# Kernel tuning notes

Measured on AMD Instinct MI355X. Metric: run time of the kernel, lower is better.

The kernel has to match this reference:

```python
import jax, jax.numpy as jnp
import numpy as np

EMBED = 1024
HEADS = 16


def setup_inputs() -> dict:
    key = jax.random.key(0)
    k1, k2, k3 = jax.random.split(key, 3)
    b, n, e = 2, 2048, EMBED
    x = jax.random.normal(k1, (b, n, e), dtype=jnp.float32)
    # torch nn.Linear stores weight as [out_features, in_features]
    w_qkv = jax.random.normal(k2, (3 * e, e), dtype=jnp.float32) * (1.0 / np.sqrt(e))
    w_proj = jax.random.normal(k3, (e, e), dtype=jnp.float32) * (1.0 / np.sqrt(e))
    b_proj = jnp.zeros((e,), dtype=jnp.float32)
    return {"x": x, "w_qkv": w_qkv, "w_proj": w_proj, "b_proj": b_proj}


def reference(x, w_qkv, w_proj, b_proj):
    b, n, e = x.shape
    h = HEADS
    d = e // h
    # qkv: [b, n, 3e]; einops 'b n (h d qkv)' -> qkv index is innermost
    qkv = jnp.einsum('bne,fe->bnf', x, w_qkv).reshape(b, n, h, d, 3)
    # -> [b, h, n, d] each
    q = jnp.transpose(qkv[..., 0], (0, 2, 1, 3))
    k = jnp.transpose(qkv[..., 1], (0, 2, 1, 3))
    v = jnp.transpose(qkv[..., 2], (0, 2, 1, 3))
    energy = jnp.einsum('bhqd,bhkd->bhqk', q, k)
    # NOTE: original applies softmax first, THEN divides by sqrt(embed_size)
    scaling = jnp.asarray(e, dtype=x.dtype) ** 0.5
    att = jax.nn.softmax(energy, axis=-1) / scaling
    out = jnp.einsum('bhqk,bhkd->bhqd', att, v)
    out = jnp.transpose(out, (0, 2, 1, 3)).reshape(b, n, e)
    proj = jnp.einsum('bne,fe->bnf', out, w_proj) + b_proj
    return jax.nn.relu(proj)
```

## Files before the change

### kernel.cpp

```cpp
#include <hip/hip_runtime.h>
#include <math.h>

constexpr int EMBED = 1024;
constexpr int HEADS = 16;
constexpr int HDIM  = 64;
constexpr int BATCH = 2;
constexpr int SEQ   = 2048;
constexpr int MTOT  = BATCH * SEQ;
constexpr int LDA   = 1024;
constexpr int BHSZ  = SEQ * HDIM;

typedef unsigned short u16;
using f16x8  = __attribute__((ext_vector_type(8))) short;
using f32x4  = __attribute__((ext_vector_type(4))) float;
using f32x16 = __attribute__((ext_vector_type(16))) float;
using u32x4  = __attribute__((ext_vector_type(4))) unsigned int;

__device__ __forceinline__ u16 f2bf(float f) {
    unsigned u = __builtin_bit_cast(unsigned, f);
    return (u16)((u + 0x7fffu + ((u >> 16) & 1u)) >> 16);
}
__device__ __forceinline__ u16 f2h(float f) {
    _Float16 h = (_Float16)f;
    return __builtin_bit_cast(u16, h);
}
__device__ __forceinline__ unsigned cvtpk(float lo, float hi) {
    unsigned r;
    asm("v_cvt_pk_bf16_f32 %0, %1, %2" : "=v"(r) : "v"(lo), "v"(hi));
    return r;
}
__device__ __forceinline__ float exp2i(float x) {
    float r;
    asm("v_exp_f32 %0, %1" : "=v"(r) : "v"(x));
    return r;
}

#define GLOAD16(gp, lp) __builtin_amdgcn_global_load_lds( \
    (const __attribute__((address_space(1))) unsigned int*)(gp), \
    (__attribute__((address_space(3))) unsigned int*)(lp), 16, 0, 0)

__global__ __launch_bounds__(256)
void convert_split(const float* __restrict__ X, const float* __restrict__ Wq,
                   const float* __restrict__ Wp,
                   u16* __restrict__ Xs, u16* __restrict__ Wqs, u16* __restrict__ Wps)
{
    int m = blockIdx.x;
    int k = threadIdx.x * 4;
    const float* src; u16* dst;
    if (m < 4096) {
        src = X + (size_t)m * EMBED;          dst = Xs + (size_t)m * LDA;
    } else if (m < 7168) {
        int f = m - 4096;
        int h = f / 192, rem = f - h * 192, d = rem / 3, wq = rem - d * 3;
        int nrow = wq * 1024 + h * 64 + d;
        src = Wq + (size_t)f * EMBED;         dst = Wqs + (size_t)nrow * LDA;
    } else {
        int lm = m - 7168;
        src = Wp + (size_t)lm * EMBED;        dst = Wps + (size_t)lm * LDA;
    }
    float4 v = *(const float4*)(src + k);
    ushort4 hv;
    hv.x = f2h(v.x); hv.y = f2h(v.y); hv.z = f2h(v.z); hv.w = f2h(v.w);
    *(ushort4*)(dst + k) = hv;
}

__device__ __forceinline__ void stage4(
    const u16* __restrict__ A, const u16* __restrict__ B,
    u16* SHu, int buf, int kt, int tid)
{
    const int k0 = kt * 32;
    u16* dst = SHu + buf * 16384;
    #pragma unroll
    for (int i = 0; i < 2; ++i) {
        const int s    = i * 512 + tid;
        const int row  = s >> 2;
        const int gcol = ((s & 3) ^ ((row >> 1) & 3)) * 8;
        GLOAD16(A + (size_t)row * LDA + k0 + gcol, dst + s * 8);
        GLOAD16(B + (size_t)row * LDA + k0 + gcol, dst + 8192 + s * 8);
    }
}

__global__ __launch_bounds__(512)
void gemm_qkv_pipe(const u16* __restrict__ Xs, const u16* __restrict__ Wqs,
                   u16* __restrict__ Qh, u16* __restrict__ Kh,
                   u16* __restrict__ Vt)
{
    __shared__ __align__(16) u16 SHu[65536];
    const int bid = blockIdx.x;
    const int xcd = bid & 7, j = bid >> 3;
    const int bm  = xcd * 2 + (j & 1);
    const int bn  = j >> 1;
    const int tid = threadIdx.x, wid = tid >> 6, lane = tid & 63;
    const int wr  = wid >> 2, wc = wid & 3;

    const u16* Ab = Xs  + (size_t)bm * 256 * LDA;
    const u16* Bb = Wqs + (size_t)bn * 256 * LDA;

    const int frow = lane & 15;
    const int kg8s = ((lane >> 4) ^ ((lane >> 1) & 3)) * 8;

    f32x4 acc[8][4] = {};

    stage4(Ab, Bb, SHu, 0, 0, tid);
    stage4(Ab, Bb, SHu, 1, 1, tid);
    stage4(Ab, Bb, SHu, 2, 2, tid);
    asm volatile("s_waitcnt vmcnt(8)" ::: "memory");
    __builtin_amdgcn_s_barrier();

    for (int kt = 0; kt < 32; ++kt) {
        const u16* bufp = SHu + (kt & 3) * 16384;
        f16x8 bf[4], af[8];
        #pragma unroll
        for (int ni = 0; ni < 4; ++ni)
            bf[ni] = *(const f16x8*)&bufp[8192 + (wc * 64 + ni * 16 + frow) * 32 + kg8s];
        #pragma unroll
        for (int mi = 0; mi < 8; ++mi)
            af[mi] = *(const f16x8*)&bufp[(wr * 128 + mi * 16 + frow) * 32 + kg8s];
        if (kt + 3 < 32) stage4(Ab, Bb, SHu, (kt + 3) & 3, kt + 3, tid);
        __builtin_amdgcn_s_setprio(1);
        #pragma unroll
        for (int mi = 0; mi < 8; ++mi)
            #pragma unroll
            for (int ni = 0; ni < 4; ++ni)
                acc[mi][ni] = __builtin_amdgcn_mfma_f32_16x16x32_f16(
                    af[mi], bf[ni], acc[mi][ni], 0, 0, 0);
        __builtin_amdgcn_s_setprio(0);
        asm volatile("s_waitcnt lgkmcnt(0)" ::: "memory");
        if (kt <= 28) { asm volatile("s_waitcnt vmcnt(8)" ::: "memory"); }
        else          { asm volatile("s_waitcnt vmcnt(0)" ::: "memory"); }
        __builtin_amdgcn_s_barrier();
    }

    const int f_base = bn * 256 + wc * 64;
    const int which  = f_base >> 10;
    const int h      = (f_base >> 6) & 15;
    char* T = (char*)(SHu + wid * 8192);
    constexpr float RCP_LN2 = 1.4426950408889634f;

    #pragma unroll
    for (int hp = 0; hp < 2; ++hp) {
        const int ng  = bm * 256 + wr * 128 + hp * 64;
        const int b_  = ng >> 11;
        const int n0w = ng & 2047;
        const size_t bhb = (size_t)(b_ * HEADS + h) * BHSZ;

        if (which < 2) {
            const float qs = (which == 0) ? RCP_LN2 : 1.0f;
            u16* dst = (which == 0 ? Qh : Kh) + bhb;
            #pragma unroll
            for (int mi = 0; mi < 4; ++mi)
                #pragma unroll
                for (int ni = 0; ni < 4; ++ni)
                    #pragma unroll
                    for (int r = 0; r < 4; ++r) {
                        u16 ov = f2h(acc[hp * 4 + mi][ni][r] * qs);
                        int nl = ((lane >> 4) << 2) + mi * 16 + r;
                        int dl = ni * 16 + (lane & 15);
                        *(u16*)(T + nl * 128 + ((dl * 2) ^ ((nl & 7) << 4))) = ov;
                    }
            #pragma unroll
            for (int t2 = 0; t2 < 2; ++t2)
                #pragma unroll
                for (int dt = 0; dt < 4; ++dt) {
                    int nl   = t2 * 32 + (lane & 31);
                    int doff = (dt * 16 + (lane >> 5) * 8) * 2;
                    f16x8 fr = *(const f16x8*)(T + nl * 128 + (doff ^ ((nl & 7) << 4)));
                    int tile = (n0w >> 5) + t2;
                    *(f16x8*)&dst[(size_t)(tile * 4 + dt) * 512 + lane * 8] = fr;
                }
        } else {
            #pragma unroll
            for (int mi = 0; mi < 4; ++mi)
                #pragma unroll
                for (int ni = 0; ni < 4; ++ni)
                    #pragma unroll
                    for (int r = 0; r < 4; ++r) {
                        int nl = ((lane >> 4) << 2) + mi * 16 + r;
                        int dl = ni * 16 + (lane & 15);
                        *(u16*)(T + nl * 128 + ((dl * 2) ^ ((nl & 7) << 4))) =
                            f2bf(acc[hp * 4 + mi][ni][r]);
                    }
            u16* dst = Vt + bhb;
            #pragma unroll
            for (int t2 = 0; t2 < 2; ++t2)
                #pragma unroll
                for (int dtv = 0; dtv < 2; ++dtv)
                    #pragma unroll
                    for (int kt2 = 0; kt2 < 2; ++kt2) {
                        int dcol = (dtv * 32 + (lane & 31)) * 2;
                        int nb   = t2 * 32 + kt2 * 16 + (lane >> 5) * 8;
                        f16x8 fr;
                        #pragma unroll
                        for (int j2 = 0; j2 < 8; ++j2) {
                            int nl = nb + j2;
                            fr[j2] = *(const short*)(T + nl * 128 + (dcol ^ ((nl & 7) << 4)));
                        }
                        int tile = (n0w >> 5) + t2;
                        *(f16x8*)&dst[(size_t)(((tile * 2 + dtv) * 2 + kt2) * 64 + lane) * 8] = fr;
                    }
        }
    }
}

__device__ __forceinline__ void stage_pf(
    const u16* __restrict__ A, const u16* __restrict__ B,
    u16* As, u16* Bs, int buf, int t, int wid, int lane)
{
    const int k0 = t * 32;
    const int srow = lane >> 2;
    const int sc   = (((lane & 3) ^ ((lane >> 3) & 3))) * 8;
    u16* ab = As + buf * 4096;
    u16* bb = Bs + buf * 4096;
    #pragma unroll
    for (int i = 0; i < 2; ++i) {
        const int rb = wid * 32 + i * 16;
        GLOAD16(A + (size_t)(rb + srow) * LDA + k0 + sc, ab + rb * 32);
        GLOAD16(B + (size_t)(rb + srow) * LDA + k0 + sc, bb + rb * 32);
    }
}

__device__ __forceinline__ void mfma_loop_pf(
    const u16* __restrict__ Ab, const u16* __restrict__ Bb,
    u16* As, u16* Bs, f32x4 (&acc)[4][4], int wid, int lane)
{
    constexpr int NT = 32;
    const int wr = wid >> 1, wc = wid & 1;
    const int frow = lane & 15;
    const int kg8s = (((lane >> 4) ^ ((lane >> 1) & 3))) * 8;

    stage_pf(Ab, Bb, As, Bs, 0, 0, wid, lane);
    stage_pf(Ab, Bb, As, Bs, 1, 1, wid, lane);
    asm volatile("s_waitcnt vmcnt(4)" ::: "memory");
    __builtin_amdgcn_s_barrier();
    __builtin_amdgcn_sched_barrier(0);

    int cb = 0, sb = 2;
    for (int t = 0; t < NT; ++t) {
        if (t + 2 < NT) stage_pf(Ab, Bb, As, Bs, sb, t + 2, wid, lane);
        const u16* ap = As + cb * 4096;
        const u16* bp = Bs + cb * 4096;
        f16x8 a[4], b[4];
        #pragma unroll
        for (int mi = 0; mi < 4; ++mi)
            a[mi] = *(const f16x8*)&ap[(wr * 64 + mi * 16 + frow) * 32 + kg8s];
        #pragma unroll
        for (int ni = 0; ni < 4; ++ni)
            b[ni] = *(const f16x8*)&bp[(wc * 64 + ni * 16 + frow) * 32 + kg8s];
        #pragma unroll
        for (int mi = 0; mi < 4; ++mi)
            #pragma unroll
            for (int ni = 0; ni < 4; ++ni)
                acc[mi][ni] = __builtin_amdgcn_mfma_f32_16x16x32_f16(
                    a[mi], b[ni], acc[mi][ni], 0, 0, 0);
        __builtin_amdgcn_sched_barrier(0);
        asm volatile("s_waitcnt lgkmcnt(0)" ::: "memory");
        if (t + 2 < NT) { asm volatile("s_waitcnt vmcnt(4)" ::: "memory"); }
        else            { asm volatile("s_waitcnt vmcnt(0)" ::: "memory"); }
        __builtin_amdgcn_s_barrier();
        __builtin_amdgcn_sched_barrier(0);
        cb = cb == 2 ? 0 : cb + 1;
        sb = sb == 2 ? 0 : sb + 1;
    }
}

__global__ __launch_bounds__(256)
void gemm_proj_mfma(const u16* __restrict__ CTXs, const u16* __restrict__ Wps,
                    const float* __restrict__ bias, float* __restrict__ Out)
{
    __shared__ __align__(16) u16 SH[6 * 4096];
    const int bid = blockIdx.x;
    const int xcd = bid & 7, j = bid >> 3;
    const int bm  = xcd * 4 + (j & 3);
    const int bn  = j >> 2;
    const int wid = threadIdx.x >> 6, lane = threadIdx.x & 63;
    const int wr = wid >> 1, wc = wid & 1;

    f32x4 acc[4][4] = {};
    mfma_loop_pf(CTXs + (size_t)bm * 128 * LDA, Wps + (size_t)bn * 128 * LDA,
                 SH, SH + 3 * 4096, acc, wid, lane);

    const int m0 = bm * 128 + wr * 64 + ((lane >> 4) << 2);
    #pragma unroll
    for (int ni = 0; ni < 4; ++ni) {
        const int f  = bn * 128 + wc * 64 + ni * 16 + (lane & 15);
        const float bv = bias[f];
        #pragma unroll
        for (int mi = 0; mi < 4; ++mi) {
            const int m = m0 + mi * 16;
            #pragma unroll
            for (int r = 0; r < 4; ++r)
                Out[(size_t)(m + r) * EMBED + f] = fmaxf(acc[mi][ni][r] + bv, 0.f);
        }
    }
}

__device__ __forceinline__ void attn_body(
    int t, int tend,
    const u16* __restrict__ vb, const u16* __restrict__ kb,
    f16x8 (&kfc)[4], f16x8 (&kfn)[4],
    f16x8 (&vfc)[4], f16x8 (&vfn)[4],
    const f16x8 (&qf)[4],
    f32x16& ot0, f32x16& ot1, float& l_run)
{
    if (t + 1 < tend) {
        #pragma unroll
        for (int dt = 0; dt < 4; ++dt)
            kfn[dt] = *(const f16x8*)(kb + (size_t)(t + 1) * 2048 + dt * 512);
        #pragma unroll
        for (int dt = 0; dt < 2; ++dt)
            #pragma unroll
            for (int kt = 0; kt < 2; ++kt)
                vfn[dt * 2 + kt] = *(const f16x8*)(vb + (size_t)(t + 1) * 2048 + dt * 1024 + kt * 512);
    }

    f32x16 st = {-16.f, -16.f, -16.f, -16.f, -16.f, -16.f, -16.f, -16.f,
                 -16.f, -16.f, -16.f, -16.f, -16.f, -16.f, -16.f, -16.f};
    #pragma unroll
    for (int dt = 0; dt < 4; ++dt)
        st = __builtin_amdgcn_mfma_f32_32x32x16_f16(kfc[dt], qf[dt], st, 0, 0, 0);

    float p[16];
    #pragma unroll
    for (int r = 0; r < 16; ++r) p[r] = exp2i(st[r]);
    {
        float s0 = (p[0] + p[1]) + (p[2] + p[3]);
        float s1 = (p[4] + p[5]) + (p[6] + p[7]);
        float s2 = (p[8] + p[9]) + (p[10] + p[11]);
        float s3 = (p[12] + p[13]) + (p[14] + p[15]);
        l_run += (s0 + s1) + (s2 + s3);
    }

    unsigned W0 = cvtpk(p[0],  p[1]),  W1 = cvtpk(p[2],  p[3]);
    unsigned W2 = cvtpk(p[4],  p[5]),  W3 = cvtpk(p[6],  p[7]);
    unsigned W4 = cvtpk(p[8],  p[9]),  W5 = cvtpk(p[10], p[11]);
    unsigned W6 = cvtpk(p[12], p[13]), W7 = cvtpk(p[14], p[15]);
    asm("v_permlane32_swap_b32 %0, %1" : "+v"(W0), "+v"(W2));
    asm("v_permlane32_swap_b32 %0, %1" : "+v"(W1), "+v"(W3));
    asm("v_permlane32_swap_b32 %0, %1" : "+v"(W4), "+v"(W6));
    asm("v_permlane32_swap_b32 %0, %1" : "+v"(W5), "+v"(W7));
    u32x4 u0 = {W0, W1, W2, W3};
    u32x4 u1 = {W4, W5, W6, W7};
    f16x8 pf0 = __builtin_bit_cast(f16x8, u0);
    f16x8 pf1 = __builtin_bit_cast(f16x8, u1);

    ot0 = __builtin_amdgcn_mfma_f32_32x32x16_bf16(vfc[0], pf0, ot0, 0, 0, 0);
    ot1 = __builtin_amdgcn_mfma_f32_32x32x16_bf16(vfc[2], pf0, ot1, 0, 0, 0);
    ot0 = __builtin_amdgcn_mfma_f32_32x32x16_bf16(vfc[1], pf1, ot0, 0, 0, 0);
    ot1 = __builtin_amdgcn_mfma_f32_32x32x16_bf16(vfc[3], pf1, ot1, 0, 0, 0);
}

__global__ __launch_bounds__(256)
void attn_mfma(const u16* __restrict__ Qh, const u16* __restrict__ Kh,
               const u16* __restrict__ Vt,  u16* __restrict__ CTXs)
{
    __shared__ __align__(16) float Lot[2][64][33];
    __shared__ float Lml[2][32];
    __shared__ __align__(16) float Ol[2][32][68];

    const int bid  = blockIdx.x;
    const int swz  = (bid & 7) * 128 + (bid >> 3);
    const int bh   = swz >> 5;
    const int qp   = swz & 31;
    const int wid  = threadIdx.x >> 6;
    const int lane = threadIdx.x & 63;
    const int col  = lane & 31;
    const int g    = lane >> 5;
    const int qt   = wid >> 1;
    const int kh   = wid & 1;

    const int q0   = qp * 64 + qt * 32;
    const int b_   = bh / HEADS;
    const int h    = bh % HEADS;
    const int tbeg = kh * (SEQ / 2 / 32);
    const int tend = tbeg + SEQ / 2 / 32;

    const size_t bhb = (size_t)bh * BHSZ;
    const u16* kb = Kh + bhb + (size_t)lane * 8;
    const u16* vb = Vt + bhb + (size_t)lane * 8;

    f16x8 qf[4];
    {
        const u16* qbh = Qh + bhb + (size_t)(q0 >> 5) * 2048 + (size_t)lane * 8;
        #pragma unroll
        for (int dt = 0; dt < 4; ++dt)
            qf[dt] = *(const f16x8*)(qbh + dt * 512);
    }

    f32x16 ot0 = {}, ot1 = {};
    float l_run = 0.0f;

    f16x8 kfA[4], kfB[4], vfA[4], vfB[4];
    #pragma unroll
    for (int dt = 0; dt < 4; ++dt)
        kfA[dt] = *(const f16x8*)(kb + (size_t)tbeg * 2048 + dt * 512);
    #pragma unroll
    for (int dt = 0; dt < 2; ++dt)
        #pragma unroll
        for (int kt = 0; kt < 2; ++kt)
            vfA[dt * 2 + kt] = *(const f16x8*)(vb + (size_t)tbeg * 2048 + dt * 1024 + kt * 512);

    for (int t = tbeg; t < tend; t += 2) {
        attn_body(t,     tend, vb, kb, kfA, kfB, vfA, vfB, qf, ot0, ot1, l_run);
        attn_body(t + 1, tend, vb, kb, kfB, kfA, vfB, vfA, qf, ot0, ot1, l_run);
    }

    l_run += __shfl_xor(l_run, 32);

    if (kh == 1) {
        #pragma unroll
        for (int r = 0; r < 16; ++r) {
            int d = (r & 3) + 8 * (r >> 2) + 4 * g;
            Lot[qt][d][col]      = ot0[r];
            Lot[qt][d + 32][col] = ot1[r];
        }
        if (g == 0) Lml[qt][col] = l_run;
    }
    __syncthreads();
    if (kh == 0) {
        float l  = l_run + Lml[qt][col];
        float sc = 1.0f / (l * 32.0f);
        #pragma unroll
        for (int r = 0; r < 16; ++r) {
            int d = (r & 3) + 8 * (r >> 2) + 4 * g;
            Ol[qt][col][d]      = (ot0[r] + Lot[qt][d][col]) * sc;
            Ol[qt][col][d + 32] = (ot1[r] + Lot[qt][d + 32][col]) * sc;
        }
        #pragma unroll
        for (int pass = 0; pass < 8; ++pass) {
            int qq = pass * 4 + (lane >> 4);
            int dd = (lane & 15) * 4;
            float4 t = *(const float4*)&Ol[qt][qq][dd];
            int m_ = b_ * SEQ + q0 + qq;
            ushort4 hv;
            hv.x = f2h(t.x); hv.y = f2h(t.y);
            hv.z = f2h(t.z); hv.w = f2h(t.w);
            *(ushort4*)&CTXs[(size_t)m_ * LDA + h * HDIM + dd] = hv;
        }
    }
}

extern "C" void kernel_launch(void* const* d_in, const int* in_sizes, int n_in,
                              void* d_out, int out_size, void* d_ws, size_t ws_size,
                              hipStream_t stream)
{
    const float* x      = (const float*)d_in[0];
    const float* w_qkv  = (const float*)d_in[1];
    const float* w_proj = (const float*)d_in[2];
    const float* b_proj = (const float*)d_in[3];
    float* out = (float*)d_out;

    const size_t seg = (size_t)BATCH * HEADS * SEQ * HDIM;
    char* w = (char*)d_ws;
    u16* Xs   = (u16*)w;  w += (size_t)MTOT * LDA * 2;
    u16* Wqs  = (u16*)w;  w += (size_t)3 * EMBED * LDA * 2;
    u16* Wps  = (u16*)w;  w += (size_t)EMBED * LDA * 2;
    u16* Qh   = (u16*)w;  w += seg * 2;
    u16* Kh   = (u16*)w;  w += seg * 2;
    u16* Vt   = (u16*)w;  w += seg * 2;
    u16* CTXs = Xs;

    convert_split<<<dim3(8192), 256, 0, stream>>>(x, w_qkv, w_proj, Xs, Wqs, Wps);
    gemm_qkv_pipe<<<dim3(192), 512, 0, stream>>>(Xs, Wqs, Qh, Kh, Vt);
    attn_mfma<<<dim3(1024), 256, 0, stream>>>(Qh, Kh, Vt, CTXs);
    gemm_proj_mfma<<<dim3(256), 256, 0, stream>>>(CTXs, Wps, b_proj, out);
}
```

Measured before the change: 112.3 us.

## Process two query tiles per attention wave to reuse K/V fragments

Each attention wave now computes scores and outputs for two 32-query tiles against the same K and V fragments, so each K/V global load is reused twice. The grid is halved to 512 blocks and the block-to-(head, query) swizzle is adjusted. The split-K reduction epilogue runs twice with extra barriers. This doubles accumulator and Q register usage and halves the number of blocks, which can lower occupancy and latency hiding.

```diff
diff --git a/kernel.cpp b/kernel.cpp
--- a/kernel.cpp
+++ b/kernel.cpp
@@ -299,8 +299,9 @@
     const u16* __restrict__ vb, const u16* __restrict__ kb,
     f16x8 (&kfc)[4], f16x8 (&kfn)[4],
     f16x8 (&vfc)[4], f16x8 (&vfn)[4],
-    const f16x8 (&qf)[4],
-    f32x16& ot0, f32x16& ot1, float& l_run)
+    const f16x8 (&qfa)[4], const f16x8 (&qfb)[4],
+    f32x16& oa0, f32x16& oa1, f32x16& ob0, f32x16& ob1,
+    float& la, float& lb)
 {
     if (t + 1 < tend) {
         #pragma unroll
@@ -313,40 +314,63 @@
                 vfn[dt * 2 + kt] = *(const f16x8*)(vb + (size_t)(t + 1) * 2048 + dt * 1024 + kt * 512);
     }
 
-    f32x16 st = {-16.f, -16.f, -16.f, -16.f, -16.f, -16.f, -16.f, -16.f,
-                 -16.f, -16.f, -16.f, -16.f, -16.f, -16.f, -16.f, -16.f};
-    #pragma unroll
-    for (int dt = 0; dt < 4; ++dt)
-        st = __builtin_amdgcn_mfma_f32_32x32x16_f16(kfc[dt], qf[dt], st, 0, 0, 0);
-
-    float p[16];
-    #pragma unroll
-    for (int r = 0; r < 16; ++r) p[r] = exp2i(st[r]);
+    const f32x16 minit = {-16.f, -16.f, -16.f, -16.f, -16.f, -16.f, -16.f, -16.f,
+                          -16.f, -16.f, -16.f, -16.f, -16.f, -16.f, -16.f, -16.f};
+    f32x16 sta = minit, stb = minit;
+    #pragma unroll
+    for (int dt = 0; dt < 4; ++dt) {
+        sta = __builtin_amdgcn_mfma_f32_32x32x16_f16(kfc[dt], qfa[dt], sta, 0, 0, 0);
+        stb = __builtin_amdgcn_mfma_f32_32x32x16_f16(kfc[dt], qfb[dt], stb, 0, 0, 0);
+    }
+
+    f16x8 pa0, pa1, pb0, pb1;
     {
-        float s0 = (p[0] + p[1]) + (p[2] + p[3]);
-        float s1 = (p[4] + p[5]) + (p[6] + p[7]);
-        float s2 = (p[8] + p[9]) + (p[10] + p[11]);
-        float s3 = (p[12] + p[13]) + (p[14] + p[15]);
-        l_run += (s0 + s1) + (s2 + s3);
-    }
-
-    unsigned W0 = cvtpk(p[0],  p[1]),  W1 = cvtpk(p[2],  p[3]);
-    unsigned W2 = cvtpk(p[4],  p[5]),  W3 = cvtpk(p[6],  p[7]);
-    unsigned W4 = cvtpk(p[8],  p[9]),  W5 = cvtpk(p[10], p[11]);
-    unsigned W6 = cvtpk(p[12], p[13]), W7 = cvtpk(p[14], p[15]);
-    asm("v_permlane32_swap_b32 %0, %1" : "+v"(W0), "+v"(W2));
-    asm("v_permlane32_swap_b32 %0, %1" : "+v"(W1), "+v"(W3));
-    asm("v_permlane32_swap_b32 %0, %1" : "+v"(W4), "+v"(W6));
-    asm("v_permlane32_swap_b32 %0, %1" : "+v"(W5), "+v"(W7));
-    u32x4 u0 = {W0, W1, W2, W3};
-    u32x4 u1 = {W4, W5, W6, W7};
-    f16x8 pf0 = __builtin_bit_cast(f16x8, u0);
-    f16x8 pf1 = __builtin_bit_cast(f16x8, u1);
-
-    ot0 = __builtin_amdgcn_mfma_f32_32x32x16_bf16(vfc[0], pf0, ot0, 0, 0, 0);
-    ot1 = __builtin_amdgcn_mfma_f32_32x32x16_bf16(vfc[2], pf0, ot1, 0, 0, 0);
-    ot0 = __builtin_amdgcn_mfma_f32_32x32x16_bf16(vfc[1], pf1, ot0, 0, 0, 0);
-    ot1 = __builtin_amdgcn_mfma_f32_32x32x16_bf16(vfc[3], pf1, ot1, 0, 0, 0);
+        float p[16];
+        #pragma unroll
+        for (int r = 0; r < 16; ++r) p[r] = exp2i(sta[r]);
+        la += ((p[0] + p[1]) + (p[2] + p[3])) + ((p[4] + p[5]) + (p[6] + p[7]))
+            + ((p[8] + p[9]) + (p[10] + p[11])) + ((p[12] + p[13]) + (p[14] + p[15]));
+        unsigned W0 = cvtpk(p[0],  p[1]),  W1 = cvtpk(p[2],  p[3]);
+        unsigned W2 = cvtpk(p[4],  p[5]),  W3 = cvtpk(p[6],  p[7]);
+        unsigned W4 = cvtpk(p[8],  p[9]),  W5 = cvtpk(p[10], p[11]);
+        unsigned W6 = cvtpk(p[12], p[13]), W7 = cvtpk(p[14], p[15]);
+        asm("v_permlane32_swap_b32 %0, %1" : "+v"(W0), "+v"(W2));
+        asm("v_permlane32_swap_b32 %0, %1" : "+v"(W1), "+v"(W3));
+        asm("v_permlane32_swap_b32 %0, %1" : "+v"(W4), "+v"(W6));
+        asm("v_permlane32_swap_b32 %0, %1" : "+v"(W5), "+v"(W7));
+        u32x4 u0 = {W0, W1, W2, W3};
+        u32x4 u1 = {W4, W5, W6, W7};
+        pa0 = __builtin_bit_cast(f16x8, u0);
+        pa1 = __builtin_bit_cast(f16x8, u1);
+    }
+    {
+        float p[16];
+        #pragma unroll
+        for (int r = 0; r < 16; ++r) p[r] = exp2i(stb[r]);
+        lb += ((p[0] + p[1]) + (p[2] + p[3])) + ((p[4] + p[5]) + (p[6] + p[7]))
+            + ((p[8] + p[9]) + (p[10] + p[11])) + ((p[12] + p[13]) + (p[14] + p[15]));
+        unsigned W0 = cvtpk(p[0],  p[1]),  W1 = cvtpk(p[2],  p[3]);
+        unsigned W2 = cvtpk(p[4],  p[5]),  W3 = cvtpk(p[6],  p[7]);
+        unsigned W4 = cvtpk(p[8],  p[9]),  W5 = cvtpk(p[10], p[11]);
+        unsigned W6 = cvtpk(p[12], p[13]), W7 = cvtpk(p[14], p[15]);
+        asm("v_permlane32_swap_b32 %0, %1" : "+v"(W0), "+v"(W2));
+        asm("v_permlane32_swap_b32 %0, %1" : "+v"(W1), "+v"(W3));
+        asm("v_permlane32_swap_b32 %0, %1" : "+v"(W4), "+v"(W6));
+        asm("v_permlane32_swap_b32 %0, %1" : "+v"(W5), "+v"(W7));
+        u32x4 u0 = {W0, W1, W2, W3};
+        u32x4 u1 = {W4, W5, W6, W7};
+        pb0 = __builtin_bit_cast(f16x8, u0);
+        pb1 = __builtin_bit_cast(f16x8, u1);
+    }
+
+    oa0 = __builtin_amdgcn_mfma_f32_32x32x16_bf16(vfc[0], pa0, oa0, 0, 0, 0);
+    oa1 = __builtin_amdgcn_mfma_f32_32x32x16_bf16(vfc[2], pa0, oa1, 0, 0, 0);
+    ob0 = __builtin_amdgcn_mfma_f32_32x32x16_bf16(vfc[0], pb0, ob0, 0, 0, 0);
+    ob1 = __builtin_amdgcn_mfma_f32_32x32x16_bf16(vfc[2], pb0, ob1, 0, 0, 0);
+    oa0 = __builtin_amdgcn_mfma_f32_32x32x16_bf16(vfc[1], pa1, oa0, 0, 0, 0);
+    oa1 = __builtin_amdgcn_mfma_f32_32x32x16_bf16(vfc[3], pa1, oa1, 0, 0, 0);
+    ob0 = __builtin_amdgcn_mfma_f32_32x32x16_bf16(vfc[1], pb1, ob0, 0, 0, 0);
+    ob1 = __builtin_amdgcn_mfma_f32_32x32x16_bf16(vfc[3], pb1, ob1, 0, 0, 0);
 }
 
 __global__ __launch_bounds__(256)
@@ -358,9 +382,9 @@
     __shared__ __align__(16) float Ol[2][32][68];
 
     const int bid  = blockIdx.x;
-    const int swz  = (bid & 7) * 128 + (bid >> 3);
-    const int bh   = swz >> 5;
-    const int qp   = swz & 31;
+    const int swz  = (bid & 7) * 64 + (bid >> 3);
+    const int bh   = swz >> 4;
+    const int qp   = swz & 15;
     const int wid  = threadIdx.x >> 6;
     const int lane = threadIdx.x & 63;
     const int col  = lane & 31;
@@ -368,7 +392,7 @@
     const int qt   = wid >> 1;
     const int kh   = wid & 1;
 
-    const int q0   = qp * 64 + qt * 32;
+    const int q0   = qp * 128 + qt * 64;
     const int b_   = bh / HEADS;
     const int h    = bh % HEADS;
     const int tbeg = kh * (SEQ / 2 / 32);
@@ -378,16 +402,18 @@
     const u16* kb = Kh + bhb + (size_t)lane * 8;
     const u16* vb = Vt + bhb + (size_t)lane * 8;
 
-    f16x8 qf[4];
+    f16x8 qfa[4], qfb[4];
     {
-        const u16* qbh = Qh + bhb + (size_t)(q0 >> 5) * 2048 + (size_t)lane * 8;
-        #pragma unroll
-        for (int dt = 0; dt < 4; ++dt)
-            qf[dt] = *(const f16x8*)(qbh + dt * 512);
-    }
-
-    f32x16 ot0 = {}, ot1 = {};
-    float l_run = 0.0f;
+        const u16* qb0 = Qh + bhb + (size_t)(q0 >> 5) * 2048 + (size_t)lane * 8;
+        #pragma unroll
+        for (int dt = 0; dt < 4; ++dt) {
+            qfa[dt] = *(const f16x8*)(qb0 + dt * 512);
+            qfb[dt] = *(const f16x8*)(qb0 + 2048 + dt * 512);
+        }
+    }
+
+    f32x16 oa0 = {}, oa1 = {}, ob0 = {}, ob1 = {};
+    float la = 0.0f, lb = 0.0f;
 
     f16x8 kfA[4], kfB[4], vfA[4], vfB[4];
     #pragma unroll
@@ -400,41 +426,49 @@
             vfA[dt * 2 + kt] = *(const f16x8*)(vb + (size_t)tbeg * 2048 + dt * 1024 + kt * 512);
 
     for (int t = tbeg; t < tend; t += 2) {
-        attn_body(t,     tend, vb, kb, kfA, kfB, vfA, vfB, qf, ot0, ot1, l_run);
-        attn_body(t + 1, tend, vb, kb, kfB, kfA, vfB, vfA, qf, ot0, ot1, l_run);
-    }
-
-    l_run += __shfl_xor(l_run, 32);
-
-    if (kh == 1) {
-        #pragma unroll
-        for (int r = 0; r < 16; ++r) {
-            int d = (r & 3) + 8 * (r >> 2) + 4 * g;
-            Lot[qt][d][col]      = ot0[r];
-            Lot[qt][d + 32][col] = ot1[r];
+        attn_body(t,     tend, vb, kb, kfA, kfB, vfA, vfB, qfa, qfb, oa0, oa1, ob0, ob1, la, lb);
+        attn_body(t + 1, tend, vb, kb, kfB, kfA, vfB, vfA, qfa, qfb, oa0, oa1, ob0, ob1, la, lb);
+    }
+
+    la += __shfl_xor(la, 32);
+    lb += __shfl_xor(lb, 32);
+
+    #pragma unroll
+    for (int sub = 0; sub < 2; ++sub) {
+        const f32x16& s0 = sub ? ob0 : oa0;
+        const f32x16& s1 = sub ? ob1 : oa1;
+        const float   ls = sub ? lb  : la;
+        __syncthreads();
+        if (kh == 1) {
+            #pragma unroll
+            for (int r = 0; r < 16; ++r) {
+                int d = (r & 3) + 8 * (r >> 2) + 4 * g;
+                Lot[qt][d][col]      = s0[r];
+                Lot[qt][d + 32][col] = s1[r];
+            }
+            if (g == 0) Lml[qt][col] = ls;
         }
-        if (g == 0) Lml[qt][col] = l_run;
-    }
-    __syncthreads();
-    if (kh == 0) {
-        float l  = l_run + Lml[qt][col];
-        float sc = 1.0f / (l * 32.0f);
-        #pragma unroll
-        for (int r = 0; r < 16; ++r) {
-            int d = (r & 3) + 8 * (r >> 2) + 4 * g;
-            Ol[qt][col][d]      = (ot0[r] + Lot[qt][d][col]) * sc;
-            Ol[qt][col][d + 32] = (ot1[r] + Lot[qt][d + 32][col]) * sc;
-        }
-        #pragma unroll
-        for (int pass = 0; pass < 8; ++pass) {
-            int qq = pass * 4 + (lane >> 4);
-            int dd = (lane & 15) * 4;
-            float4 t = *(const float4*)&Ol[qt][qq][dd];
-            int m_ = b_ * SEQ + q0 + qq;
-            ushort4 hv;
-            hv.x = f2h(t.x); hv.y = f2h(t.y);
-            hv.z = f2h(t.z); hv.w = f2h(t.w);
-            *(ushort4*)&CTXs[(size_t)m_ * LDA + h * HDIM + dd] = hv;
+        __syncthreads();
+        if (kh == 0) {
+            float l  = ls + Lml[qt][col];
+            float sc = 1.0f / (l * 32.0f);
+            #pragma unroll
+            for (int r = 0; r < 16; ++r) {
+                int d = (r & 3) + 8 * (r >> 2) + 4 * g;
+                Ol[qt][col][d]      = (s0[r] + Lot[qt][d][col]) * sc;
+                Ol[qt][col][d + 32] = (s1[r] + Lot[qt][d + 32][col]) * sc;
+            }
+            #pragma unroll
+            for (int pass = 0; pass < 8; ++pass) {
+                int qq = pass * 4 + (lane >> 4);
+                int dd = (lane & 15) * 4;
+                float4 t = *(const float4*)&Ol[qt][qq][dd];
+                int m_ = b_ * SEQ + q0 + sub * 32 + qq;
+                ushort4 hv;
+                hv.x = f2h(t.x); hv.y = f2h(t.y);
+                hv.z = f2h(t.z); hv.w = f2h(t.w);
+                *(ushort4*)&CTXs[(size_t)m_ * LDA + h * HDIM + dd] = hv;
+            }
         }
     }
 }
@@ -461,6 +495,6 @@
 
     convert_split<<<dim3(8192), 256, 0, stream>>>(x, w_qkv, w_proj, Xs, Wqs, Wps);
     gemm_qkv_pipe<<<dim3(192), 512, 0, stream>>>(Xs, Wqs, Qh, Kh, Vt);
-    attn_mfma<<<dim3(1024), 256, 0, stream>>>(Qh, Kh, Vt, CTXs);
+    attn_mfma<<<dim3(512), 256, 0, stream>>>(Qh, Kh, Vt, CTXs);
     gemm_proj_mfma<<<dim3(256), 256, 0, stream>>>(CTXs, Wps, b_proj, out);
 }
```

After: 110.7 us. About the same (-1.4%).

## Software-pipeline attention loop: overlap next QK^T with current PV and softmax

Applied to the files above, without the earlier changes.

Restructures the attention inner loop so that each step issues the QK^T MFMAs for tile i+1 together with the PV MFMAs for tile i, then computes the softmax of tile i+1 after issuing the next global loads. K is prefetched two tiles ahead and V one tile ahead. s_setprio raises wave priority around the MFMA block. The aim is to hide the exp/convert/permlane softmax latency and the load latency behind matrix work. The cost is more live registers (two P fragments, extra K/V buffers), which may lower occupancy or cause spills.

```diff
diff --git a/kernel.cpp b/kernel.cpp
--- a/kernel.cpp
+++ b/kernel.cpp
@@ -294,42 +294,14 @@
     }
 }
 
-__device__ __forceinline__ void attn_body(
-    int t, int tend,
-    const u16* __restrict__ vb, const u16* __restrict__ kb,
-    f16x8 (&kfc)[4], f16x8 (&kfn)[4],
-    f16x8 (&vfc)[4], f16x8 (&vfn)[4],
-    const f16x8 (&qf)[4],
-    f32x16& ot0, f32x16& ot1, float& l_run)
-{
-    if (t + 1 < tend) {
-        #pragma unroll
-        for (int dt = 0; dt < 4; ++dt)
-            kfn[dt] = *(const f16x8*)(kb + (size_t)(t + 1) * 2048 + dt * 512);
-        #pragma unroll
-        for (int dt = 0; dt < 2; ++dt)
-            #pragma unroll
-            for (int kt = 0; kt < 2; ++kt)
-                vfn[dt * 2 + kt] = *(const f16x8*)(vb + (size_t)(t + 1) * 2048 + dt * 1024 + kt * 512);
-    }
-
-    f32x16 st = {-16.f, -16.f, -16.f, -16.f, -16.f, -16.f, -16.f, -16.f,
-                 -16.f, -16.f, -16.f, -16.f, -16.f, -16.f, -16.f, -16.f};
-    #pragma unroll
-    for (int dt = 0; dt < 4; ++dt)
-        st = __builtin_amdgcn_mfma_f32_32x32x16_f16(kfc[dt], qf[dt], st, 0, 0, 0);
-
+__device__ __forceinline__ void attn_softmax(
+    const f32x16& st, f16x8 (&pf)[2], float& l_run)
+{
     float p[16];
     #pragma unroll
     for (int r = 0; r < 16; ++r) p[r] = exp2i(st[r]);
-    {
-        float s0 = (p[0] + p[1]) + (p[2] + p[3]);
-        float s1 = (p[4] + p[5]) + (p[6] + p[7]);
-        float s2 = (p[8] + p[9]) + (p[10] + p[11]);
-        float s3 = (p[12] + p[13]) + (p[14] + p[15]);
-        l_run += (s0 + s1) + (s2 + s3);
-    }
-
+    l_run += ((p[0] + p[1]) + (p[2] + p[3])) + ((p[4] + p[5]) + (p[6] + p[7]))
+           + ((p[8] + p[9]) + (p[10] + p[11])) + ((p[12] + p[13]) + (p[14] + p[15]));
     unsigned W0 = cvtpk(p[0],  p[1]),  W1 = cvtpk(p[2],  p[3]);
     unsigned W2 = cvtpk(p[4],  p[5]),  W3 = cvtpk(p[6],  p[7]);
     unsigned W4 = cvtpk(p[8],  p[9]),  W5 = cvtpk(p[10], p[11]);
@@ -340,13 +312,51 @@
     asm("v_permlane32_swap_b32 %0, %1" : "+v"(W5), "+v"(W7));
     u32x4 u0 = {W0, W1, W2, W3};
     u32x4 u1 = {W4, W5, W6, W7};
-    f16x8 pf0 = __builtin_bit_cast(f16x8, u0);
-    f16x8 pf1 = __builtin_bit_cast(f16x8, u1);
-
-    ot0 = __builtin_amdgcn_mfma_f32_32x32x16_bf16(vfc[0], pf0, ot0, 0, 0, 0);
-    ot1 = __builtin_amdgcn_mfma_f32_32x32x16_bf16(vfc[2], pf0, ot1, 0, 0, 0);
-    ot0 = __builtin_amdgcn_mfma_f32_32x32x16_bf16(vfc[1], pf1, ot0, 0, 0, 0);
-    ot1 = __builtin_amdgcn_mfma_f32_32x32x16_bf16(vfc[3], pf1, ot1, 0, 0, 0);
+    pf[0] = __builtin_bit_cast(f16x8, u0);
+    pf[1] = __builtin_bit_cast(f16x8, u1);
+}
+
+__device__ __forceinline__ void attn_step(
+    int i, int tbeg,
+    const u16* __restrict__ vb, const u16* __restrict__ kb,
+    f16x8 (&kNext)[4], f16x8 (&vCur)[4],
+    const f16x8 (&qf)[4],
+    f16x8 (&pfCur)[2], f16x8 (&pfNext)[2],
+    f32x16& ot0, f32x16& ot1, float& l_run)
+{
+    const bool doQK = (i + 1) < 32;
+    const f32x16 minit = {-16.f, -16.f, -16.f, -16.f, -16.f, -16.f, -16.f, -16.f,
+                          -16.f, -16.f, -16.f, -16.f, -16.f, -16.f, -16.f, -16.f};
+    f32x16 st = minit;
+
+    __builtin_amdgcn_s_setprio(1);
+    if (doQK) {
+        #pragma unroll
+        for (int dt = 0; dt < 4; ++dt)
+            st = __builtin_amdgcn_mfma_f32_32x32x16_f16(kNext[dt], qf[dt], st, 0, 0, 0);
+    }
+    ot0 = __builtin_amdgcn_mfma_f32_32x32x16_bf16(vCur[0], pfCur[0], ot0, 0, 0, 0);
+    ot1 = __builtin_amdgcn_mfma_f32_32x32x16_bf16(vCur[2], pfCur[0], ot1, 0, 0, 0);
+    ot0 = __builtin_amdgcn_mfma_f32_32x32x16_bf16(vCur[1], pfCur[1], ot0, 0, 0, 0);
+    ot1 = __builtin_amdgcn_mfma_f32_32x32x16_bf16(vCur[3], pfCur[1], ot1, 0, 0, 0);
+    __builtin_amdgcn_s_setprio(0);
+
+    if (i + 3 < 32) {
+        const size_t t3 = (size_t)(tbeg + i + 3) * 2048;
+        #pragma unroll
+        for (int dt = 0; dt < 4; ++dt)
+            kNext[dt] = *(const f16x8*)(kb + t3 + dt * 512);
+    }
+    if (i + 2 < 32) {
+        const size_t t2 = (size_t)(tbeg + i + 2) * 2048;
+        #pragma unroll
+        for (int dt = 0; dt < 2; ++dt)
+            #pragma unroll
+            for (int kt = 0; kt < 2; ++kt)
+                vCur[dt * 2 + kt] = *(const f16x8*)(vb + t2 + dt * 1024 + kt * 512);
+    }
+
+    if (doQK) attn_softmax(st, pfNext, l_run);
 }
 
 __global__ __launch_bounds__(256)
@@ -371,8 +381,7 @@
     const int q0   = qp * 64 + qt * 32;
     const int b_   = bh / HEADS;
     const int h    = bh % HEADS;
-    const int tbeg = kh * (SEQ / 2 / 32);
-    const int tend = tbeg + SEQ / 2 / 32;
+    const int tbeg = kh * 32;
 
     const size_t bhb = (size_t)bh * BHSZ;
     const u16* kb = Kh + bhb + (size_t)lane * 8;
@@ -389,19 +398,39 @@
     f32x16 ot0 = {}, ot1 = {};
     float l_run = 0.0f;
 
-    f16x8 kfA[4], kfB[4], vfA[4], vfB[4];
-    #pragma unroll
-    for (int dt = 0; dt < 4; ++dt)
-        kfA[dt] = *(const f16x8*)(kb + (size_t)tbeg * 2048 + dt * 512);
-    #pragma unroll
-    for (int dt = 0; dt < 2; ++dt)
-        #pragma unroll
-        for (int kt = 0; kt < 2; ++kt)
-            vfA[dt * 2 + kt] = *(const f16x8*)(vb + (size_t)tbeg * 2048 + dt * 1024 + kt * 512);
-
-    for (int t = tbeg; t < tend; t += 2) {
-        attn_body(t,     tend, vb, kb, kfA, kfB, vfA, vfB, qf, ot0, ot1, l_run);
-        attn_body(t + 1, tend, vb, kb, kfB, kfA, vfB, vfA, qf, ot0, ot1, l_run);
+    f16x8 kA[4], kB[4], vA[4], vB[4], pfA[2], pfB[2];
+    {
+        const size_t t0 = (size_t)tbeg * 2048;
+        #pragma unroll
+        for (int dt = 0; dt < 4; ++dt) {
+            kA[dt] = *(const f16x8*)(kb + t0 + dt * 512);
+            kB[dt] = *(const f16x8*)(kb + t0 + 2048 + dt * 512);
+        }
+        #pragma unroll
+        for (int dt = 0; dt < 2; ++dt)
+            #pragma unroll
+            for (int kt = 0; kt < 2; ++kt) {
+                vA[dt * 2 + kt] = *(const f16x8*)(vb + t0 + dt * 1024 + kt * 512);
+                vB[dt * 2 + kt] = *(const f16x8*)(vb + t0 + 2048 + dt * 1024 + kt * 512);
+            }
+    }
+    {
+        const f32x16 minit = {-16.f, -16.f, -16.f, -16.f, -16.f, -16.f, -16.f, -16.f,
+                              -16.f, -16.f, -16.f, -16.f, -16.f, -16.f, -16.f, -16.f};
+        f32x16 st = minit;
+        #pragma unroll
+        for (int dt = 0; dt < 4; ++dt)
+            st = __builtin_amdgcn_mfma_f32_32x32x16_f16(kA[dt], qf[dt], st, 0, 0, 0);
+        const size_t t2 = (size_t)(tbeg + 2) * 2048;
+        #pragma unroll
+        for (int dt = 0; dt < 4; ++dt)
+            kA[dt] = *(const f16x8*)(kb + t2 + dt * 512);
+        attn_softmax(st, pfA, l_run);
+    }
+
+    for (int i = 0; i < 32; i += 2) {
+        attn_step(i,     tbeg, vb, kb, kB, vA, qf, pfA, pfB, ot0, ot1, l_run);
+        attn_step(i + 1, tbeg, vb, kb, kA, vB, qf, pfB, pfA, ot0, ot1, l_run);
     }
 
     l_run += __shfl_xor(l_run, 32);
```

Measured after the change: 112.8 us. About the same (+0.4%).
